# Kernel tuning notes

Hardware: AMD Instinct MI355X
Metric: run time of the kernel (lower is better)

The kernel has to match this reference:

```python
import jax, jax.numpy as jnp
import numpy as np

D_MODEL = 768
NUM_HEADS = 12
HEAD_DIM = D_MODEL // NUM_HEADS
D_FF = 3072
LN_EPS = 1e-5


def _xavier(key, shape):
    # nn.init.xavier_uniform_ on a [out, in] Linear weight
    fan_out, fan_in = shape[-2], shape[-1]
    limit = float(np.sqrt(6.0 / (fan_in + fan_out)))
    return jax.random.uniform(key, shape, jnp.float32, -limit, limit)


def setup_inputs() -> dict:
    key = jax.random.key(0)
    ks = jax.random.split(key, 10)
    x = jax.random.normal(ks[0], (4, 2048, D_MODEL), jnp.float32)
    # per-head projections stacked: [H, head_dim, d_model] (torch Linear weight layout [out, in])
    Wq = _xavier(ks[1], (NUM_HEADS, HEAD_DIM, D_MODEL))
    Wk = _xavier(ks[2], (NUM_HEADS, HEAD_DIM, D_MODEL))
    Wv = _xavier(ks[3], (NUM_HEADS, HEAD_DIM, D_MODEL))
    Wo = _xavier(ks[4], (D_MODEL, D_MODEL))
    W1 = jax.random.normal(ks[5], (D_FF, D_MODEL), jnp.float32) * 0.02
    b1 = jnp.zeros((D_FF,), jnp.float32)
    W2 = jax.random.normal(ks[6], (D_MODEL, D_FF), jnp.float32) * 0.02
    b2 = jnp.zeros((D_MODEL,), jnp.float32)
    g1 = jnp.ones((D_MODEL,), jnp.float32)
    be1 = jnp.zeros((D_MODEL,), jnp.float32)
    g2 = jnp.ones((D_MODEL,), jnp.float32)
    be2 = jnp.zeros((D_MODEL,), jnp.float32)
    return {"x": x, "Wq": Wq, "Wk": Wk, "Wv": Wv, "Wo": Wo,
            "W1": W1, "b1": b1, "W2": W2, "b2": b2,
            "g1": g1, "be1": be1, "g2": g2, "be2": be2}


def _layernorm(x, g, b):
    mu = jnp.mean(x, axis=-1, keepdims=True)
    var = jnp.mean(jnp.square(x - mu), axis=-1, keepdims=True)
    return (x - mu) * jax.lax.rsqrt(var + LN_EPS) * g + b


def reference(x, Wq, Wk, Wv, Wo, W1, b1, W2, b2, g1, be1, g2, be2):
    B, S, D = x.shape
    # all heads batched (same math as the per-head Python loop + concat)
    q = jnp.einsum('bsd,hed->bhse', x, Wq)   # [B,H,S,e]
    k = jnp.einsum('bsd,hed->bhse', x, Wk)
    v = jnp.einsum('bsd,hed->bhse', x, Wv)
    scores = jnp.einsum('bhse,bhte->bhst', q, k) / jnp.sqrt(jnp.float32(HEAD_DIM))
    attn = jax.nn.softmax(scores, axis=-1)
    ctx = jnp.einsum('bhst,bhte->bhse', attn, v)
    # concat heads along feature dim (head order matches stacking order)
    concat = ctx.transpose(0, 2, 1, 3).reshape(B, S, D)
    attn_out = concat @ Wo.T
    h = _layernorm(x + attn_out, g1, be1)
    ffn = jax.nn.relu(h @ W1.T + b1) @ W2.T + b2
    out = _layernorm(h + ffn, g2, be2)
    return out
```

## Files before the change

### kernel.cpp

```cpp
#include <hip/hip_runtime.h>

typedef unsigned short u16;
typedef unsigned int u32;
typedef __attribute__((ext_vector_type(8))) short short8;
typedef __attribute__((ext_vector_type(4))) float f32x4;
typedef __attribute__((ext_vector_type(4))) unsigned short u16x4;

extern "C" __device__ float __ocml_native_exp2_f32(float);
#define EXP2(x) __ocml_native_exp2_f32(x)

__device__ __forceinline__ float b2f(u16 u){
  union { float f; unsigned int i; } c; c.i = ((unsigned int)u) << 16; return c.f;
}
__device__ __forceinline__ u16 f2b(float f){
  union { float f; unsigned int i; } c; c.f = f;
  unsigned int i = c.i;
  unsigned int r = (i + 0x7FFFu + ((i >> 16) & 1u)) >> 16;
  return (u16)r;
}

#define GLD16(gp, lp) __builtin_amdgcn_global_load_lds( \
    (const __attribute__((address_space(1))) void*)(gp), \
    (__attribute__((address_space(3))) void*)(lp), 16, 0, 0)

__device__ __forceinline__ u32 pkbf(float lo, float hi){
  u32 r;
  asm volatile("v_cvt_pk_bf16_f32 %0, %1, %2" : "=v"(r) : "v"(lo), "v"(hi));
  return r;
}

__global__ __launch_bounds__(256) void cvt_all(
    const float* __restrict__ s0, const float* __restrict__ s1,
    const float* __restrict__ s2, const float* __restrict__ s3,
    const float* __restrict__ s4, const float* __restrict__ s5,
    const float* __restrict__ s6, u16* __restrict__ dst)
{
  const int i = (blockIdx.x * 256 + threadIdx.x) * 4;
  const float* sp;
  if      (i <  6291456) sp = s0 + i;
  else if (i <  6881280) sp = s1 + (i - 6291456);
  else if (i <  7471104) sp = s2 + (i - 6881280);
  else if (i <  8060928) sp = s3 + (i - 7471104);
  else if (i <  8650752) sp = s4 + (i - 8060928);
  else if (i < 11010048) sp = s5 + (i - 8650752);
  else                   sp = s6 + (i - 11010048);
  float4 f = *(const float4*)sp;
  u16x4 o = { f2b(f.x), f2b(f.y), f2b(f.z), f2b(f.w) };
  *(u16x4*)(dst + i) = o;
}

enum { EPI_QKV = 0, EPI_WO = 1, EPI_FFN1 = 2, EPI_FFN2 = 3 };
__device__ __forceinline__ float KSCALE_C(){ return 0.125f * 1.44269504088896340736f; }

template<int EPI>
__global__ __launch_bounds__(256) void gemm_bt(
    const u16* __restrict__ A, const u16* __restrict__ Bm,
    int K, int gx,
    u16* __restrict__ outB,
    const float* __restrict__ auxF,
    const u16* __restrict__ auxB)
{
  __shared__ __align__(16) short Asm[2][128][32];
  __shared__ __align__(16) short Bsm[2][128][32];
  const int tid  = threadIdx.x;
  const int lane = tid & 63;
  const int wid  = tid >> 6;
  const int wr = wid >> 1, wc = wid & 1;
  const int fr = lane & 15, fq = lane >> 4;

  const int nwg = gridDim.x;
  const int lin = blockIdx.x;
  const int wg  = (lin & 7) * (nwg >> 3) + (lin >> 3);
  const int bx = wg % gx, by = wg / gx;
  const int m0 = by * 128, n0 = bx * 128;

  f32x4 acc[4][4];
#pragma unroll
  for (int i = 0; i < 4; i++)
#pragma unroll
    for (int j = 0; j < 4; j++) acc[i][j] = (f32x4){0.f, 0.f, 0.f, 0.f};

  const int lrow = lane >> 2;
  const int sc   = (((lane & 3) ^ ((lrow >> 1) & 3))) << 3;
  const int rc   = ((fq ^ ((fr >> 1) & 3))) << 3;

#define GSTAGE(b, kt) do { \
    const u16* ga_ = A  + (size_t)(m0 + wid*32 + lrow) * K + (kt)*32 + sc; \
    const u16* gb_ = Bm + (size_t)(n0 + wid*32 + lrow) * K + (kt)*32 + sc; \
    GLD16(ga_,                 &Asm[b][wid*32][0]); \
    GLD16(ga_ + (size_t)16*K,  &Asm[b][wid*32 + 16][0]); \
    GLD16(gb_,                 &Bsm[b][wid*32][0]); \
    GLD16(gb_ + (size_t)16*K,  &Bsm[b][wid*32 + 16][0]); \
  } while(0)

  const int NT = K >> 5;
  GSTAGE(0, 0);
  __syncthreads();

  int bufn = 0;
  for (int kt = 0; kt < NT; ++kt) {
    if (kt + 1 < NT) GSTAGE(bufn ^ 1, kt + 1);
    short8 a[4], b[4];
#pragma unroll
    for (int i = 0; i < 4; i++) a[i] = *(const short8*)&Asm[bufn][wr*64 + i*16 + fr][rc];
#pragma unroll
    for (int j = 0; j < 4; j++) b[j] = *(const short8*)&Bsm[bufn][wc*64 + j*16 + fr][rc];
    __builtin_amdgcn_s_setprio(1);
#pragma unroll
    for (int i = 0; i < 4; i++)
#pragma unroll
      for (int j = 0; j < 4; j++)
        acc[i][j] = __builtin_amdgcn_mfma_f32_16x16x32_bf16(a[i], b[j], acc[i][j], 0, 0, 0);
    __builtin_amdgcn_s_setprio(0);
    __syncthreads();
    bufn ^= 1;
  }
#undef GSTAGE

#pragma unroll
  for (int i = 0; i < 4; i++) {
    const int row0 = m0 + wr*64 + i*16 + fq*4;
#pragma unroll
    for (int j = 0; j < 4; j++) {
      const int col = n0 + wc*64 + j*16 + fr;
#pragma unroll
      for (int r = 0; r < 4; r++) {
        const int row = row0 + r;
        float val = acc[i][j][r];
        if (EPI == EPI_QKV) {
          int tt = (col >= 1536) ? 2 : (col >= 768 ? 1 : 0);
          int rem = col - tt * 768;
          int h = rem >> 6, e = rem & 63;
          int bb = row >> 11, s = row & 2047;
          if (tt == 2) {
            size_t idx = (((size_t)(bb*12 + h)) * 64 + e) * 2048 + s;
            ((u16*)auxB)[idx] = f2b(val);
          } else {
            size_t idx = (((size_t)(tt*48 + bb*12 + h)) * 2048 + s) * 64 + e;
            if (tt == 1) val *= KSCALE_C();
            outB[idx] = f2b(val);
          }
        } else {
          float o = val + auxF[col];
          o = o > 0.f ? o : 0.f;
          outB[(size_t)row * 3072 + col] = f2b(o);
        }
      }
    }
  }
}

template<int EPI>
__global__ __launch_bounds__(256) void gemm_n64(
    const u16* __restrict__ A, const u16* __restrict__ Bm,
    int K,
    u16* __restrict__ outB,
    const float* __restrict__ auxF,
    const u16* __restrict__ auxB)
{
  __shared__ __align__(16) short Asm[2][128][32];
  __shared__ __align__(16) short Bsm[2][64][32];
  const int tid  = threadIdx.x;
  const int lane = tid & 63;
  const int wid  = tid >> 6;
  const int wr = wid >> 1, wc = wid & 1;
  const int fr = lane & 15, fq = lane >> 4;

  const int nwg = gridDim.x;
  const int lin = blockIdx.x;
  const int wg  = (lin & 7) * (nwg >> 3) + (lin >> 3);
  const int bx = wg % 12, by = wg / 12;
  const int m0 = by * 128, n0 = bx * 64;

  f32x4 acc[4][2];
#pragma unroll
  for (int i = 0; i < 4; i++)
#pragma unroll
    for (int j = 0; j < 2; j++) acc[i][j] = (f32x4){0.f, 0.f, 0.f, 0.f};

  const int lrow = lane >> 2;
  const int sc   = (((lane & 3) ^ ((lrow >> 1) & 3))) << 3;
  const int rc   = ((fq ^ ((fr >> 1) & 3))) << 3;

#define GSTAGE(b, kt) do { \
    const u16* ga_ = A  + (size_t)(m0 + wid*32 + lrow) * K + (kt)*32 + sc; \
    const u16* gb_ = Bm + (size_t)(n0 + wid*16 + lrow) * K + (kt)*32 + sc; \
    GLD16(ga_,                 &Asm[b][wid*32][0]); \
    GLD16(ga_ + (size_t)16*K,  &Asm[b][wid*32 + 16][0]); \
    GLD16(gb_,                 &Bsm[b][wid*16][0]); \
  } while(0)

  const int NT = K >> 5;
  GSTAGE(0, 0);
  __syncthreads();

  int bufn = 0;
  for (int kt = 0; kt < NT; ++kt) {
    if (kt + 1 < NT) GSTAGE(bufn ^ 1, kt + 1);
    short8 a[4], b[2];
#pragma unroll
    for (int i = 0; i < 4; i++) a[i] = *(const short8*)&Asm[bufn][wr*64 + i*16 + fr][rc];
#pragma unroll
    for (int j = 0; j < 2; j++) b[j] = *(const short8*)&Bsm[bufn][wc*32 + j*16 + fr][rc];
    __builtin_amdgcn_s_setprio(1);
#pragma unroll
    for (int i = 0; i < 4; i++)
#pragma unroll
      for (int j = 0; j < 2; j++)
        acc[i][j] = __builtin_amdgcn_mfma_f32_16x16x32_bf16(a[i], b[j], acc[i][j], 0, 0, 0);
    __builtin_amdgcn_s_setprio(0);
    __syncthreads();
    bufn ^= 1;
  }
#undef GSTAGE

#pragma unroll
  for (int i = 0; i < 4; i++) {
    const int row0 = m0 + wr*64 + i*16 + fq*4;
#pragma unroll
    for (int j = 0; j < 2; j++) {
      const int col = n0 + wc*32 + j*16 + fr;
#pragma unroll
      for (int r = 0; r < 4; r++) {
        const int row = row0 + r;
        float val = acc[i][j][r];
        size_t idx = (size_t)row * 768 + col;
        if (EPI == EPI_WO) {
          outB[idx] = f2b(val + b2f(auxB[idx]));
        } else {
          outB[idx] = f2b(val + auxF[col] + b2f(auxB[idx]));
        }
      }
    }
  }
}

__global__ __launch_bounds__(512) void flash_attn(
    const u16* __restrict__ q, const u16* __restrict__ kmat, const u16* __restrict__ vtmat,
    u16* __restrict__ ctx)
{
  const int tid = threadIdx.x;
  const int lane = tid & 63, wid = tid >> 6;
  const int fr = lane & 15, fq = lane >> 4;
  const int orig = blockIdx.x;
  const int wg = (orig & 7) * 96 + (orig >> 3);
  const int qb = wg & 15;
  const int ph = wg >> 4;
  const size_t plane = (size_t)ph * 2048 * 64;
  const u16* qp  = q + plane;
  const u16* kp  = kmat + plane;
  const u16* vtp = vtmat + plane;

  __shared__ __align__(16) short Ksm[2][64][64];
  __shared__ __align__(16) short Vsm[2][64][64];

  const int qr0 = qb*128 + wid*16;
  const short8 aq0 = *(const short8*)(qp + (size_t)(qr0 + fr)*64 + fq*8);
  const short8 aq1 = *(const short8*)(qp + (size_t)(qr0 + fr)*64 + 32 + fq*8);

  short8 vones;
#pragma unroll
  for (int j = 0; j < 8; j++) vones[j] = (short)0x3F80;

  const int rA = wid*8 + (lane >> 3);
  const int cA = (((lane & 7) ^ ((rA & 3) | (((rA >> 3) & 1) << 2)))) * 8;

#define STAGE(B, KT) do { \
    GLD16(kp  + (size_t)((KT)*64 + rA)*64 + cA,  &Ksm[B][wid*8][0]); \
    GLD16(vtp + (size_t)rA*2048 + (KT)*64 + cA,  &Vsm[B][wid*8][0]); \
  } while(0)

  f32x4 o[4];
#pragma unroll
  for (int eb = 0; eb < 4; eb++) o[eb] = (f32x4){0.f, 0.f, 0.f, 0.f};
  float m = -1e30f, l = 0.f;
  const f32x4 zero = (f32x4){0.f, 0.f, 0.f, 0.f};

  STAGE(0, 0);
  __syncthreads();

  const int fK  = (fr & 3) | (((fr >> 2) & 1) << 2);
  const int kc0 = ((fq    ) ^ fK) * 8;
  const int kc1 = ((4 + fq) ^ fK) * 8;
  const int krow = (fr & 3) + 8 * (fr >> 2);
  const int fV  = (fr & 3) | (((fr >> 3) & 1) << 2);
  const int vc0 = ((fq    ) ^ fV) * 8;
  const int vc1 = ((4 + fq) ^ fV) * 8;

  int buf = 0;
  for (int kt = 0; kt < 32; ++kt) {
    if (kt < 31) STAGE(buf ^ 1, kt + 1);

    f32x4 st[2][2];
    __builtin_amdgcn_s_setprio(1);
#pragma unroll
    for (int h = 0; h < 2; h++)
#pragma unroll
      for (int c = 0; c < 2; c++) {
        const short* kr = &Ksm[buf][32*h + 4*c + krow][0];
        short8 kf0 = *(const short8*)(kr + kc0);
        short8 kf1 = *(const short8*)(kr + kc1);
        f32x4 a = __builtin_amdgcn_mfma_f32_16x16x32_bf16(kf0, aq0, zero, 0, 0, 0);
        st[h][c]  = __builtin_amdgcn_mfma_f32_16x16x32_bf16(kf1, aq1, a,    0, 0, 0);
      }
    __builtin_amdgcn_s_setprio(0);

    float t0 = fmaxf(fmaxf(st[0][0][0], st[0][0][1]), st[0][0][2]);
    float t1 = fmaxf(fmaxf(st[0][0][3], st[0][1][0]), st[0][1][1]);
    float t2 = fmaxf(fmaxf(st[0][1][2], st[0][1][3]), st[1][0][0]);
    float t3 = fmaxf(fmaxf(st[1][0][1], st[1][0][2]), st[1][0][3]);
    float t4 = fmaxf(fmaxf(st[1][1][0], st[1][1][1]), st[1][1][2]);
    float u0 = fmaxf(fmaxf(t0, t1), st[1][1][3]);
    float u1 = fmaxf(fmaxf(t2, t3), t4);
    float lm = fmaxf(u0, u1);
    lm = fmaxf(lm, __shfl_xor(lm, 16));
    lm = fmaxf(lm, __shfl_xor(lm, 32));

    if (!__all(lm <= m + 8.f)) {
      float nm = fmaxf(m, lm);
      float corr = EXP2(m - nm);
      m = nm;
      l *= corr;
#pragma unroll
      for (int eb = 0; eb < 4; eb++)
#pragma unroll
        for (int r = 0; r < 4; r++) o[eb][r] *= corr;
    }

    float p[2][2][4];
#pragma unroll
    for (int h = 0; h < 2; h++)
#pragma unroll
      for (int c = 0; c < 2; c++)
#pragma unroll
        for (int r = 0; r < 4; r++)
          p[h][c][r] = EXP2(st[h][c][r] - m);

    union { u32 u[4]; short8 s8; } pf0, pf1;
    pf0.u[0] = pkbf(p[0][0][0], p[0][0][1]);
    pf0.u[1] = pkbf(p[0][0][2], p[0][0][3]);
    pf0.u[2] = pkbf(p[0][1][0], p[0][1][1]);
    pf0.u[3] = pkbf(p[0][1][2], p[0][1][3]);
    pf1.u[0] = pkbf(p[1][0][0], p[1][0][1]);
    pf1.u[1] = pkbf(p[1][0][2], p[1][0][3]);
    pf1.u[2] = pkbf(p[1][1][0], p[1][1][1]);
    pf1.u[3] = pkbf(p[1][1][2], p[1][1][3]);

    __builtin_amdgcn_s_setprio(1);
    f32x4 ol = __builtin_amdgcn_mfma_f32_16x16x32_bf16(vones, pf0.s8, zero, 0, 0, 0);
    ol       = __builtin_amdgcn_mfma_f32_16x16x32_bf16(vones, pf1.s8, ol,   0, 0, 0);
#pragma unroll
    for (int eb = 0; eb < 4; eb++) {
      const short* vr = &Vsm[buf][eb*16 + fr][0];
      o[eb] = __builtin_amdgcn_mfma_f32_16x16x32_bf16(*(const short8*)(vr + vc0), pf0.s8, o[eb], 0, 0, 0);
      o[eb] = __builtin_amdgcn_mfma_f32_16x16x32_bf16(*(const short8*)(vr + vc1), pf1.s8, o[eb], 0, 0, 0);
    }
    __builtin_amdgcn_s_setprio(0);
    l += ol[0];

    __syncthreads();
    buf ^= 1;
  }
#undef STAGE

  const float inv = 1.0f / l;
  const int s = qr0 + fr;
  u16* cp = ctx + ((size_t)((ph/12)*2048 + s)) * 768 + (ph%12)*64;
#pragma unroll
  for (int eb = 0; eb < 4; eb++) {
    u16x4 w = { f2b(o[eb][0]*inv), f2b(o[eb][1]*inv), f2b(o[eb][2]*inv), f2b(o[eb][3]*inv) };
    *(u16x4*)(cp + eb*16 + fq*4) = w;
  }
}

template<int F32OUT>
__global__ __launch_bounds__(256) void ln_k(const u16* __restrict__ in,
    const float* __restrict__ g, const float* __restrict__ be, void* __restrict__ outp)
{
  const int lane = threadIdx.x & 63, wid = threadIdx.x >> 6;
  const int row = blockIdx.x * 4 + wid;
  const u16* p = in + (size_t)row * 768;
  float v[12];
  float s = 0.f, s2 = 0.f;
#pragma unroll
  for (int i = 0; i < 6; i++) {
    ushort2 uv = *(const ushort2*)(p + i*128 + lane*2);
    v[2*i]   = b2f(uv.x);
    v[2*i+1] = b2f(uv.y);
    s += v[2*i] + v[2*i+1];
    s2 += v[2*i]*v[2*i] + v[2*i+1]*v[2*i+1];
  }
#pragma unroll
  for (int msk = 1; msk < 64; msk <<= 1) { s += __shfl_xor(s, msk); s2 += __shfl_xor(s2, msk); }
  const float mu = s * (1.f/768.f);
  const float var = s2 * (1.f/768.f) - mu*mu;
  const float rstd = rsqrtf(var + 1e-5f);
#pragma unroll
  for (int i = 0; i < 6; i++) {
    int c = i*128 + lane*2;
    float o0 = (v[2*i]   - mu) * rstd * g[c]   + be[c];
    float o1 = (v[2*i+1] - mu) * rstd * g[c+1] + be[c+1];
    if (F32OUT) {
      float2 w = { o0, o1 };
      *(float2*)((float*)outp + (size_t)row*768 + c) = w;
    } else {
      ushort2 w = { f2b(o0), f2b(o1) };
      *(ushort2*)((u16*)outp + (size_t)row*768 + c) = w;
    }
  }
}

extern "C" void kernel_launch(void* const* d_in, const int* in_sizes, int n_in,
                              void* d_out, int out_size, void* d_ws, size_t ws_size,
                              hipStream_t stream)
{
  const float* x   = (const float*)d_in[0];
  const float* Wq  = (const float*)d_in[1];
  const float* Wk  = (const float*)d_in[2];
  const float* Wv  = (const float*)d_in[3];
  const float* Wo  = (const float*)d_in[4];
  const float* W1  = (const float*)d_in[5];
  const float* b1  = (const float*)d_in[6];
  const float* W2  = (const float*)d_in[7];
  const float* b2  = (const float*)d_in[8];
  const float* g1  = (const float*)d_in[9];
  const float* be1 = (const float*)d_in[10];
  const float* g2  = (const float*)d_in[11];
  const float* be2 = (const float*)d_in[12];
  float* out = (float*)d_out;

  char* ws = (char*)d_ws;
  u16* xb     = (u16*)(ws + 0);
  u16* Wqkv_b = (u16*)(ws + 12582912);
  u16* Wo_b   = (u16*)(ws + 16121856);
  u16* W1_b   = (u16*)(ws + 17301504);
  u16* W2_b   = (u16*)(ws + 22020096);
  u16* qkv    = (u16*)(ws + 26738688);
  u16* ctxb   = (u16*)(ws + 64487424);
  u16* hidden = (u16*)(ws + 26738688);
  u16* vt     = (u16*)(ws + 77070336);
  u16* resid1 = (u16*)(ws + 77070336);
  u16* hb     = (u16*)(ws + 102236160);
  u16* pre2   = (u16*)(ws + 77070336);

  cvt_all<<<dim3(13056), 256, 0, stream>>>(x, Wq, Wk, Wv, Wo, W1, W2, (u16*)ws);

  gemm_bt<EPI_QKV><<<dim3(1152), 256, 0, stream>>>(
      xb, Wqkv_b, 768, 18, qkv, nullptr, vt);

  u16* qb_ = qkv;
  u16* kb_ = qkv + 6291456;

  flash_attn<<<dim3(768), 512, 0, stream>>>(qb_, kb_, vt, ctxb);

  gemm_n64<EPI_WO><<<dim3(768), 256, 0, stream>>>(
      ctxb, Wo_b, 768, resid1, nullptr, xb);

  ln_k<0><<<2048, 256, 0, stream>>>(resid1, g1, be1, hb);

  gemm_bt<EPI_FFN1><<<dim3(1536), 256, 0, stream>>>(
      hb, W1_b, 768, 24, hidden, b1, nullptr);

  gemm_n64<EPI_FFN2><<<dim3(768), 256, 0, stream>>>(
      hidden, W2_b, 3072, pre2, b2, hb);

  ln_k<1><<<2048, 256, 0, stream>>>(pre2, g2, be2, out);
}
```

Baseline: 302.6 us.

## Triple-buffer GEMM K-loop and give each attention wave two query tiles

The GEMM kernels move from double to triple-buffered LDS staging. Each iteration now waits with an explicit vmcnt and a single barrier instead of a trailing __syncthreads, so loads run two tiles ahead. The flash attention kernel halves its block to 256 threads, and each wave processes two 16-row query groups that share the K and V fragments it loads from LDS. This amortises LDS reads and barriers over more compute, at the cost of more registers and LDS per block.

```diff
diff --git a/kernel.cpp b/kernel.cpp
--- a/kernel.cpp
+++ b/kernel.cpp
@@ -60,8 +60,8 @@
     const float* __restrict__ auxF,
     const u16* __restrict__ auxB)
 {
-  __shared__ __align__(16) short Asm[2][128][32];
-  __shared__ __align__(16) short Bsm[2][128][32];
+  __shared__ __align__(16) short Asm[3][128][32];
+  __shared__ __align__(16) short Bsm[3][128][32];
   const int tid  = threadIdx.x;
   const int lane = tid & 63;
   const int wid  = tid >> 6;
@@ -95,16 +95,21 @@
 
   const int NT = K >> 5;
   GSTAGE(0, 0);
-  __syncthreads();
-
-  int bufn = 0;
-  for (int kt = 0; kt < NT; ++kt) {
-    if (kt + 1 < NT) GSTAGE(bufn ^ 1, kt + 1);
+  GSTAGE(1, 1);
+
+  for (int t = 0; t < NT; ++t) {
+    asm volatile("s_waitcnt vmcnt(4)" ::: "memory");
+    __builtin_amdgcn_s_barrier();
+    asm volatile("" ::: "memory");
+    const int t2 = (t + 2 < NT) ? t + 2 : NT - 1;
+    GSTAGE((t + 2) % 3, t2);
+
+    const int cur = t % 3;
     short8 a[4], b[4];
 #pragma unroll
-    for (int i = 0; i < 4; i++) a[i] = *(const short8*)&Asm[bufn][wr*64 + i*16 + fr][rc];
-#pragma unroll
-    for (int j = 0; j < 4; j++) b[j] = *(const short8*)&Bsm[bufn][wc*64 + j*16 + fr][rc];
+    for (int i = 0; i < 4; i++) a[i] = *(const short8*)&Asm[cur][wr*64 + i*16 + fr][rc];
+#pragma unroll
+    for (int j = 0; j < 4; j++) b[j] = *(const short8*)&Bsm[cur][wc*64 + j*16 + fr][rc];
     __builtin_amdgcn_s_setprio(1);
 #pragma unroll
     for (int i = 0; i < 4; i++)
@@ -112,8 +117,6 @@
       for (int j = 0; j < 4; j++)
         acc[i][j] = __builtin_amdgcn_mfma_f32_16x16x32_bf16(a[i], b[j], acc[i][j], 0, 0, 0);
     __builtin_amdgcn_s_setprio(0);
-    __syncthreads();
-    bufn ^= 1;
   }
 #undef GSTAGE
 
@@ -158,8 +161,8 @@
     const float* __restrict__ auxF,
     const u16* __restrict__ auxB)
 {
-  __shared__ __align__(16) short Asm[2][128][32];
-  __shared__ __align__(16) short Bsm[2][64][32];
+  __shared__ __align__(16) short Asm[3][128][32];
+  __shared__ __align__(16) short Bsm[3][64][32];
   const int tid  = threadIdx.x;
   const int lane = tid & 63;
   const int wid  = tid >> 6;
@@ -192,16 +195,21 @@
 
   const int NT = K >> 5;
   GSTAGE(0, 0);
-  __syncthreads();
-
-  int bufn = 0;
-  for (int kt = 0; kt < NT; ++kt) {
-    if (kt + 1 < NT) GSTAGE(bufn ^ 1, kt + 1);
+  GSTAGE(1, 1);
+
+  for (int t = 0; t < NT; ++t) {
+    asm volatile("s_waitcnt vmcnt(3)" ::: "memory");
+    __builtin_amdgcn_s_barrier();
+    asm volatile("" ::: "memory");
+    const int t2 = (t + 2 < NT) ? t + 2 : NT - 1;
+    GSTAGE((t + 2) % 3, t2);
+
+    const int cur = t % 3;
     short8 a[4], b[2];
 #pragma unroll
-    for (int i = 0; i < 4; i++) a[i] = *(const short8*)&Asm[bufn][wr*64 + i*16 + fr][rc];
-#pragma unroll
-    for (int j = 0; j < 2; j++) b[j] = *(const short8*)&Bsm[bufn][wc*32 + j*16 + fr][rc];
+    for (int i = 0; i < 4; i++) a[i] = *(const short8*)&Asm[cur][wr*64 + i*16 + fr][rc];
+#pragma unroll
+    for (int j = 0; j < 2; j++) b[j] = *(const short8*)&Bsm[cur][wc*32 + j*16 + fr][rc];
     __builtin_amdgcn_s_setprio(1);
 #pragma unroll
     for (int i = 0; i < 4; i++)
@@ -209,8 +217,6 @@
       for (int j = 0; j < 2; j++)
         acc[i][j] = __builtin_amdgcn_mfma_f32_16x16x32_bf16(a[i], b[j], acc[i][j], 0, 0, 0);
     __builtin_amdgcn_s_setprio(0);
-    __syncthreads();
-    bufn ^= 1;
   }
 #undef GSTAGE
 
@@ -235,7 +241,7 @@
   }
 }
 
-__global__ __launch_bounds__(512) void flash_attn(
+__global__ __launch_bounds__(256) void flash_attn(
     const u16* __restrict__ q, const u16* __restrict__ kmat, const u16* __restrict__ vtmat,
     u16* __restrict__ ctx)
 {
@@ -254,26 +260,36 @@
   __shared__ __align__(16) short Ksm[2][64][64];
   __shared__ __align__(16) short Vsm[2][64][64];
 
-  const int qr0 = qb*128 + wid*16;
-  const short8 aq0 = *(const short8*)(qp + (size_t)(qr0 + fr)*64 + fq*8);
-  const short8 aq1 = *(const short8*)(qp + (size_t)(qr0 + fr)*64 + 32 + fq*8);
+  const int qr0 = qb*128 + wid*32;
+  short8 aq[2][2];
+#pragma unroll
+  for (int g = 0; g < 2; g++) {
+    aq[g][0] = *(const short8*)(qp + (size_t)(qr0 + g*16 + fr)*64 + fq*8);
+    aq[g][1] = *(const short8*)(qp + (size_t)(qr0 + g*16 + fr)*64 + 32 + fq*8);
+  }
 
   short8 vones;
 #pragma unroll
   for (int j = 0; j < 8; j++) vones[j] = (short)0x3F80;
 
-  const int rA = wid*8 + (lane >> 3);
+  const int rA = wid*16 + (lane >> 3);
+  const int rB = rA + 8;
   const int cA = (((lane & 7) ^ ((rA & 3) | (((rA >> 3) & 1) << 2)))) * 8;
+  const int cB = (((lane & 7) ^ ((rB & 3) | (((rB >> 3) & 1) << 2)))) * 8;
 
 #define STAGE(B, KT) do { \
-    GLD16(kp  + (size_t)((KT)*64 + rA)*64 + cA,  &Ksm[B][wid*8][0]); \
-    GLD16(vtp + (size_t)rA*2048 + (KT)*64 + cA,  &Vsm[B][wid*8][0]); \
+    GLD16(kp  + (size_t)((KT)*64 + rA)*64 + cA,  &Ksm[B][wid*16    ][0]); \
+    GLD16(kp  + (size_t)((KT)*64 + rB)*64 + cB,  &Ksm[B][wid*16 + 8][0]); \
+    GLD16(vtp + (size_t)rA*2048 + (KT)*64 + cA,  &Vsm[B][wid*16    ][0]); \
+    GLD16(vtp + (size_t)rB*2048 + (KT)*64 + cB,  &Vsm[B][wid*16 + 8][0]); \
   } while(0)
 
-  f32x4 o[4];
-#pragma unroll
-  for (int eb = 0; eb < 4; eb++) o[eb] = (f32x4){0.f, 0.f, 0.f, 0.f};
-  float m = -1e30f, l = 0.f;
+  f32x4 o[2][4];
+#pragma unroll
+  for (int g = 0; g < 2; g++)
+#pragma unroll
+    for (int eb = 0; eb < 4; eb++) o[g][eb] = (f32x4){0.f, 0.f, 0.f, 0.f};
+  float m[2] = { -1e30f, -1e30f }, l[2] = { 0.f, 0.f };
   const f32x4 zero = (f32x4){0.f, 0.f, 0.f, 0.f};
 
   STAGE(0, 0);
@@ -291,85 +307,112 @@
   for (int kt = 0; kt < 32; ++kt) {
     if (kt < 31) STAGE(buf ^ 1, kt + 1);
 
-    f32x4 st[2][2];
-    __builtin_amdgcn_s_setprio(1);
+    short8 kf[2][2][2];
 #pragma unroll
     for (int h = 0; h < 2; h++)
 #pragma unroll
       for (int c = 0; c < 2; c++) {
         const short* kr = &Ksm[buf][32*h + 4*c + krow][0];
-        short8 kf0 = *(const short8*)(kr + kc0);
-        short8 kf1 = *(const short8*)(kr + kc1);
-        f32x4 a = __builtin_amdgcn_mfma_f32_16x16x32_bf16(kf0, aq0, zero, 0, 0, 0);
-        st[h][c]  = __builtin_amdgcn_mfma_f32_16x16x32_bf16(kf1, aq1, a,    0, 0, 0);
+        kf[h][c][0] = *(const short8*)(kr + kc0);
+        kf[h][c][1] = *(const short8*)(kr + kc1);
       }
-    __builtin_amdgcn_s_setprio(0);
-
-    float t0 = fmaxf(fmaxf(st[0][0][0], st[0][0][1]), st[0][0][2]);
-    float t1 = fmaxf(fmaxf(st[0][0][3], st[0][1][0]), st[0][1][1]);
-    float t2 = fmaxf(fmaxf(st[0][1][2], st[0][1][3]), st[1][0][0]);
-    float t3 = fmaxf(fmaxf(st[1][0][1], st[1][0][2]), st[1][0][3]);
-    float t4 = fmaxf(fmaxf(st[1][1][0], st[1][1][1]), st[1][1][2]);
-    float u0 = fmaxf(fmaxf(t0, t1), st[1][1][3]);
-    float u1 = fmaxf(fmaxf(t2, t3), t4);
-    float lm = fmaxf(u0, u1);
-    lm = fmaxf(lm, __shfl_xor(lm, 16));
-    lm = fmaxf(lm, __shfl_xor(lm, 32));
-
-    if (!__all(lm <= m + 8.f)) {
-      float nm = fmaxf(m, lm);
-      float corr = EXP2(m - nm);
-      m = nm;
-      l *= corr;
-#pragma unroll
-      for (int eb = 0; eb < 4; eb++)
-#pragma unroll
-        for (int r = 0; r < 4; r++) o[eb][r] *= corr;
-    }
-
-    float p[2][2][4];
-#pragma unroll
-    for (int h = 0; h < 2; h++)
-#pragma unroll
-      for (int c = 0; c < 2; c++)
-#pragma unroll
-        for (int r = 0; r < 4; r++)
-          p[h][c][r] = EXP2(st[h][c][r] - m);
-
-    union { u32 u[4]; short8 s8; } pf0, pf1;
-    pf0.u[0] = pkbf(p[0][0][0], p[0][0][1]);
-    pf0.u[1] = pkbf(p[0][0][2], p[0][0][3]);
-    pf0.u[2] = pkbf(p[0][1][0], p[0][1][1]);
-    pf0.u[3] = pkbf(p[0][1][2], p[0][1][3]);
-    pf1.u[0] = pkbf(p[1][0][0], p[1][0][1]);
-    pf1.u[1] = pkbf(p[1][0][2], p[1][0][3]);
-    pf1.u[2] = pkbf(p[1][1][0], p[1][1][1]);
-    pf1.u[3] = pkbf(p[1][1][2], p[1][1][3]);
-
-    __builtin_amdgcn_s_setprio(1);
-    f32x4 ol = __builtin_amdgcn_mfma_f32_16x16x32_bf16(vones, pf0.s8, zero, 0, 0, 0);
-    ol       = __builtin_amdgcn_mfma_f32_16x16x32_bf16(vones, pf1.s8, ol,   0, 0, 0);
+
+    union U { u32 u[4]; short8 s8; };
+    U pfs[2][2];
+
+#pragma unroll
+    for (int g = 0; g < 2; g++) {
+      f32x4 st[2][2];
+      __builtin_amdgcn_s_setprio(1);
+#pragma unroll
+      for (int h = 0; h < 2; h++)
+#pragma unroll
+        for (int c = 0; c < 2; c++) {
+          f32x4 a = __builtin_amdgcn_mfma_f32_16x16x32_bf16(kf[h][c][0], aq[g][0], zero, 0, 0, 0);
+          st[h][c] = __builtin_amdgcn_mfma_f32_16x16x32_bf16(kf[h][c][1], aq[g][1], a,   0, 0, 0);
+        }
+      __builtin_amdgcn_s_setprio(0);
+
+      float t0 = fmaxf(fmaxf(st[0][0][0], st[0][0][1]), st[0][0][2]);
+      float t1 = fmaxf(fmaxf(st[0][0][3], st[0][1][0]), st[0][1][1]);
+      float t2 = fmaxf(fmaxf(st[0][1][2], st[0][1][3]), st[1][0][0]);
+      float t3 = fmaxf(fmaxf(st[1][0][1], st[1][0][2]), st[1][0][3]);
+      float t4 = fmaxf(fmaxf(st[1][1][0], st[1][1][1]), st[1][1][2]);
+      float u0 = fmaxf(fmaxf(t0, t1), st[1][1][3]);
+      float u1 = fmaxf(fmaxf(t2, t3), t4);
+      float lm = fmaxf(u0, u1);
+      lm = fmaxf(lm, __shfl_xor(lm, 16));
+      lm = fmaxf(lm, __shfl_xor(lm, 32));
+
+      if (!__all(lm <= m[g] + 8.f)) {
+        float nm = fmaxf(m[g], lm);
+        float corr = EXP2(m[g] - nm);
+        m[g] = nm;
+        l[g] *= corr;
+#pragma unroll
+        for (int eb = 0; eb < 4; eb++)
+#pragma unroll
+          for (int r = 0; r < 4; r++) o[g][eb][r] *= corr;
+      }
+
+      float p[2][2][4];
+#pragma unroll
+      for (int h = 0; h < 2; h++)
+#pragma unroll
+        for (int c = 0; c < 2; c++)
+#pragma unroll
+          for (int r = 0; r < 4; r++)
+            p[h][c][r] = EXP2(st[h][c][r] - m[g]);
+
+      pfs[g][0].u[0] = pkbf(p[0][0][0], p[0][0][1]);
+      pfs[g][0].u[1] = pkbf(p[0][0][2], p[0][0][3]);
+      pfs[g][0].u[2] = pkbf(p[0][1][0], p[0][1][1]);
+      pfs[g][0].u[3] = pkbf(p[0][1][2], p[0][1][3]);
+      pfs[g][1].u[0] = pkbf(p[1][0][0], p[1][0][1]);
+      pfs[g][1].u[1] = pkbf(p[1][0][2], p[1][0][3]);
+      pfs[g][1].u[2] = pkbf(p[1][1][0], p[1][1][1]);
+      pfs[g][1].u[3] = pkbf(p[1][1][2], p[1][1][3]);
+    }
+
+    short8 vf[4][2];
 #pragma unroll
     for (int eb = 0; eb < 4; eb++) {
       const short* vr = &Vsm[buf][eb*16 + fr][0];
-      o[eb] = __builtin_amdgcn_mfma_f32_16x16x32_bf16(*(const short8*)(vr + vc0), pf0.s8, o[eb], 0, 0, 0);
-      o[eb] = __builtin_amdgcn_mfma_f32_16x16x32_bf16(*(const short8*)(vr + vc1), pf1.s8, o[eb], 0, 0, 0);
+      vf[eb][0] = *(const short8*)(vr + vc0);
+      vf[eb][1] = *(const short8*)(vr + vc1);
+    }
+
+    __builtin_amdgcn_s_setprio(1);
+    f32x4 ol[2];
+#pragma unroll
+    for (int g = 0; g < 2; g++) {
+      ol[g] = __builtin_amdgcn_mfma_f32_16x16x32_bf16(vones, pfs[g][0].s8, zero, 0, 0, 0);
+      ol[g] = __builtin_amdgcn_mfma_f32_16x16x32_bf16(vones, pfs[g][1].s8, ol[g], 0, 0, 0);
+#pragma unroll
+      for (int eb = 0; eb < 4; eb++) {
+        o[g][eb] = __builtin_amdgcn_mfma_f32_16x16x32_bf16(vf[eb][0], pfs[g][0].s8, o[g][eb], 0, 0, 0);
+        o[g][eb] = __builtin_amdgcn_mfma_f32_16x16x32_bf16(vf[eb][1], pfs[g][1].s8, o[g][eb], 0, 0, 0);
+      }
     }
     __builtin_amdgcn_s_setprio(0);
-    l += ol[0];
+    l[0] += ol[0][0];
+    l[1] += ol[1][0];
 
     __syncthreads();
     buf ^= 1;
   }
 #undef STAGE
 
-  const float inv = 1.0f / l;
-  const int s = qr0 + fr;
-  u16* cp = ctx + ((size_t)((ph/12)*2048 + s)) * 768 + (ph%12)*64;
-#pragma unroll
-  for (int eb = 0; eb < 4; eb++) {
-    u16x4 w = { f2b(o[eb][0]*inv), f2b(o[eb][1]*inv), f2b(o[eb][2]*inv), f2b(o[eb][3]*inv) };
-    *(u16x4*)(cp + eb*16 + fq*4) = w;
+#pragma unroll
+  for (int g = 0; g < 2; g++) {
+    const float inv = 1.0f / l[g];
+    const int s = qr0 + g*16 + fr;
+    u16* cp = ctx + ((size_t)((ph/12)*2048 + s)) * 768 + (ph%12)*64;
+#pragma unroll
+    for (int eb = 0; eb < 4; eb++) {
+      u16x4 w = { f2b(o[g][eb][0]*inv), f2b(o[g][eb][1]*inv), f2b(o[g][eb][2]*inv), f2b(o[g][eb][3]*inv) };
+      *(u16x4*)(cp + eb*16 + fq*4) = w;
+    }
   }
 }
 
@@ -451,7 +494,7 @@
   u16* qb_ = qkv;
   u16* kb_ = qkv + 6291456;
 
-  flash_attn<<<dim3(768), 512, 0, stream>>>(qb_, kb_, vt, ctxb);
+  flash_attn<<<dim3(768), 256, 0, stream>>>(qb_, kb_, vt, ctxb);
 
   gemm_n64<EPI_WO><<<dim3(768), 256, 0, stream>>>(
       ctxb, Wo_b, 768, resid1, nullptr, xb);
```

After: 337.8 us. 11.6% more time.
